# Optimization experiments

Hardware: AMD Instinct MI355X
Metric: run time of the kernel (lower is better)

Reference implementation:

```python
import jax, jax.numpy as jnp
import numpy as np

N = 100000      # nodes
DEG = 16        # fixed out-degree -> nnz = N*DEG (static for jit)
NNZ = N * DEG
IN_DIM, HID, OUT = 256, 64, 64


def setup_inputs() -> dict:
    key = jax.random.key(0)
    k1, k2, k3, k4, k5 = jax.random.split(key, 5)
    X = jax.random.normal(k1, (N, IN_DIM), dtype=jnp.float32)
    W1 = jax.random.normal(k2, (IN_DIM, HID), dtype=jnp.float32) / np.sqrt(IN_DIM)
    W2 = jax.random.normal(k3, (HID, OUT), dtype=jnp.float32) / np.sqrt(HID)
    vals = jax.random.uniform(k4, (NNZ,), dtype=jnp.float32)
    rowptr = (jnp.arange(N + 1, dtype=jnp.int32) * DEG)  # fixed-degree CSR
    colind = jax.random.randint(k5, (NNZ,), 0, N, dtype=jnp.int32)
    return {"X": X, "W1": W1, "W2": W2, "vals": vals,
            "rowptr": rowptr, "colind": colind}


def spmm_csr(rowptr, colind, vals, B):
    """CSR SpMM: out[i] = sum_{j in row i} vals[j] * B[colind[j]]."""
    deg = rowptr[1:] - rowptr[:-1]                      # [N]
    rows = jnp.repeat(jnp.arange(N, dtype=jnp.int32), deg,
                      total_repeat_length=NNZ)           # [NNZ]
    gathered = vals[:, None] * B[colind]                 # [NNZ, F]
    return jax.ops.segment_sum(gathered, rows, num_segments=N)


def reference(X, W1, W2, vals, rowptr, colind):
    h = X @ W1                        # lin1 (no bias)
    h = spmm_csr(rowptr, colind, vals, h)   # A @ h
    h = jax.nn.relu(h)
    out = h @ W2                      # lin2 (no bias)
    out = spmm_csr(rowptr, colind, vals, out)  # A @ out
    return out
```

## Files before the change

### kernel.cpp

```cpp
#include <hip/hip_runtime.h>

#define N_NODES 100000
#define DEG 16

typedef __attribute__((ext_vector_type(8))) short short8;
typedef __attribute__((ext_vector_type(4))) float f32x4;

__device__ inline unsigned short f2bf(float f) {
    union { float f; unsigned u; } v; v.f = f;
    unsigned u = v.u;
    u += 0x7FFFu + ((u >> 16) & 1u);
    return (unsigned short)(u >> 16);
}
__device__ inline float bflo(unsigned u) {
    union { unsigned u; float f; } v; v.u = u << 16; return v.f;
}
__device__ inline float bfhi(unsigned u) {
    union { unsigned u; float f; } v; v.u = u & 0xFFFF0000u; return v.f;
}

__global__ __launch_bounds__(256) void gemm1_k256(const float* __restrict__ X,
                                                  const float* __restrict__ W,
                                                  unsigned short* __restrict__ Y,
                                                  int M)
{
    constexpr int K = 256;
    constexpr int KPAD = K + 8;
    __shared__ unsigned short wfrag[K * 64];
    __shared__ unsigned short stage[4][16 * KPAD];

    const int tid = threadIdx.x;
    for (int idx = tid; idx < K * 64; idx += 256) {
        int j    = idx & 7;
        int lane = (idx >> 3) & 63;
        int ct   = (idx >> 9) & 3;
        int kb   = idx >> 11;
        int k    = kb * 32 + ((lane >> 4) << 3) + j;
        int col  = ct * 16 + (lane & 15);
        wfrag[idx] = f2bf(W[k * 64 + col]);
    }
    __syncthreads();

    const int lane = tid & 63;
    const int wid  = tid >> 6;
    const int q    = lane >> 4;
    const int l16  = lane & 15;
    const int rowbase = blockIdx.x * 64 + wid * 16;
    unsigned short* st = stage[wid];

    #pragma unroll
    for (int r = 0; r < 16; ++r) {
        int rg = rowbase + r; if (rg > M - 1) rg = M - 1;
        float4 x4 = *(const float4*)(X + (size_t)rg * K + lane * 4);
        ushort4 s;
        s.x = f2bf(x4.x); s.y = f2bf(x4.y); s.z = f2bf(x4.z); s.w = f2bf(x4.w);
        *(ushort4*)&st[r * KPAD + lane * 4] = s;
    }

    f32x4 acc0 = {0,0,0,0}, acc1 = {0,0,0,0}, acc2 = {0,0,0,0}, acc3 = {0,0,0,0};
    #pragma unroll
    for (int kb = 0; kb < K / 32; ++kb) {
        short8 af = *(const short8*)&st[l16 * KPAD + kb * 32 + q * 8];
        const short8* wp = (const short8*)&wfrag[((kb * 4) * 64 + lane) * 8];
        acc0 = __builtin_amdgcn_mfma_f32_16x16x32_bf16(af, wp[0 * 64], acc0, 0, 0, 0);
        acc1 = __builtin_amdgcn_mfma_f32_16x16x32_bf16(af, wp[1 * 64], acc1, 0, 0, 0);
        acc2 = __builtin_amdgcn_mfma_f32_16x16x32_bf16(af, wp[2 * 64], acc2, 0, 0, 0);
        acc3 = __builtin_amdgcn_mfma_f32_16x16x32_bf16(af, wp[3 * 64], acc3, 0, 0, 0);
    }

    unsigned short* ob = st;
    #pragma unroll
    for (int r = 0; r < 4; ++r) {
        int rr = (q * 4 + r) * 72 + l16;
        ob[rr + 0 * 16] = f2bf(acc0[r]);
        ob[rr + 1 * 16] = f2bf(acc1[r]);
        ob[rr + 2 * 16] = f2bf(acc2[r]);
        ob[rr + 3 * 16] = f2bf(acc3[r]);
    }
    #pragma unroll
    for (int i = 0; i < 4; ++i) {
        int row = i * 4 + q;
        int rg  = rowbase + row;
        if (rg < M) {
            uint2 v = *(const uint2*)&ob[row * 72 + l16 * 4];
            *(uint2*)(Y + (size_t)rg * 64 + l16 * 4) = v;
        }
    }
}

__global__ __launch_bounds__(256) void gemm2_k64(const unsigned short* __restrict__ Xb,
                                                 const float* __restrict__ W,
                                                 unsigned short* __restrict__ Y,
                                                 int M)
{
    constexpr int K = 64;
    constexpr int KPAD = K + 8;
    __shared__ unsigned short wfrag[K * 64];
    __shared__ unsigned short stage[4][16 * KPAD];

    const int tid = threadIdx.x;
    for (int idx = tid; idx < K * 64; idx += 256) {
        int j    = idx & 7;
        int lane = (idx >> 3) & 63;
        int ct   = (idx >> 9) & 3;
        int kb   = idx >> 11;
        int k    = kb * 32 + ((lane >> 4) << 3) + j;
        int col  = ct * 16 + (lane & 15);
        wfrag[idx] = f2bf(W[k * 64 + col]);
    }
    __syncthreads();

    const int lane = tid & 63;
    const int wid  = tid >> 6;
    const int q    = lane >> 4;
    const int l16  = lane & 15;
    const int rowbase = blockIdx.x * 64 + wid * 16;
    unsigned short* st = stage[wid];

    #pragma unroll
    for (int i = 0; i < 4; ++i) {
        int row = i * 4 + q;
        int rg  = rowbase + row; if (rg > M - 1) rg = M - 1;
        uint2 v = *(const uint2*)(Xb + (size_t)rg * 64 + l16 * 4);
        *(uint2*)&st[row * KPAD + l16 * 4] = v;
    }

    f32x4 acc0 = {0,0,0,0}, acc1 = {0,0,0,0}, acc2 = {0,0,0,0}, acc3 = {0,0,0,0};
    #pragma unroll
    for (int kb = 0; kb < K / 32; ++kb) {
        short8 af = *(const short8*)&st[l16 * KPAD + kb * 32 + q * 8];
        const short8* wp = (const short8*)&wfrag[((kb * 4) * 64 + lane) * 8];
        acc0 = __builtin_amdgcn_mfma_f32_16x16x32_bf16(af, wp[0 * 64], acc0, 0, 0, 0);
        acc1 = __builtin_amdgcn_mfma_f32_16x16x32_bf16(af, wp[1 * 64], acc1, 0, 0, 0);
        acc2 = __builtin_amdgcn_mfma_f32_16x16x32_bf16(af, wp[2 * 64], acc2, 0, 0, 0);
        acc3 = __builtin_amdgcn_mfma_f32_16x16x32_bf16(af, wp[3 * 64], acc3, 0, 0, 0);
    }

    unsigned short* ob = st;
    #pragma unroll
    for (int r = 0; r < 4; ++r) {
        int rr = (q * 4 + r) * 72 + l16;
        ob[rr + 0 * 16] = f2bf(acc0[r]);
        ob[rr + 1 * 16] = f2bf(acc1[r]);
        ob[rr + 2 * 16] = f2bf(acc2[r]);
        ob[rr + 3 * 16] = f2bf(acc3[r]);
    }
    #pragma unroll
    for (int i = 0; i < 4; ++i) {
        int row = i * 4 + q;
        int rg  = rowbase + row;
        if (rg < M) {
            uint2 v = *(const uint2*)&ob[row * 72 + l16 * 4];
            *(uint2*)(Y + (size_t)rg * 64 + l16 * 4) = v;
        }
    }
}

template<bool RELU, bool OUT_BF16>
__global__ __launch_bounds__(256) void spmm16_bf16(const int* __restrict__ colind,
                                                   const float* __restrict__ vals,
                                                   const unsigned short* __restrict__ B,
                                                   void* __restrict__ outp)
{
    const int tid  = threadIdx.x;
    const int lane = tid & 63;
    const int wid  = tid >> 6;
    const int q    = lane >> 4;
    const int l16  = lane & 15;
    const int row  = (blockIdx.x * 4 + wid) * 4 + q;

    const int*   ci = colind + (size_t)row * DEG;
    const float* vv = vals   + (size_t)row * DEG;

    float a0 = 0.f, a1 = 0.f, a2 = 0.f, a3 = 0.f;
    #pragma unroll
    for (int e = 0; e < DEG; ++e) {
        int   c = ci[e];
        float v = vv[e];
        uint2 b = *(const uint2*)(B + (size_t)c * 64 + l16 * 4);
        a0 += v * bflo(b.x); a1 += v * bfhi(b.x);
        a2 += v * bflo(b.y); a3 += v * bfhi(b.y);
    }
    if (RELU) {
        a0 = fmaxf(a0, 0.f); a1 = fmaxf(a1, 0.f);
        a2 = fmaxf(a2, 0.f); a3 = fmaxf(a3, 0.f);
    }
    if (OUT_BF16) {
        ushort4 o; o.x = f2bf(a0); o.y = f2bf(a1); o.z = f2bf(a2); o.w = f2bf(a3);
        *(ushort4*)((unsigned short*)outp + (size_t)row * 64 + l16 * 4) = o;
    } else {
        float4 o; o.x = a0; o.y = a1; o.z = a2; o.w = a3;
        *(float4*)((float*)outp + (size_t)row * 64 + l16 * 4) = o;
    }
}

extern "C" void kernel_launch(void* const* d_in, const int* in_sizes, int n_in,
                              void* d_out, int out_size, void* d_ws, size_t ws_size,
                              hipStream_t stream) {
    const float* X      = (const float*)d_in[0];
    const float* W1     = (const float*)d_in[1];
    const float* W2     = (const float*)d_in[2];
    const float* vals   = (const float*)d_in[3];
    const int*   colind = (const int*)d_in[5];
    float*       out    = (float*)d_out;

    unsigned short* h  = (unsigned short*)d_ws;
    unsigned short* h2 = h + (size_t)N_NODES * 64;
    unsigned short* o1 = h;

    const int gemm_grid = (N_NODES + 63) / 64;

    hipLaunchKernelGGL(gemm1_k256, dim3(gemm_grid), dim3(256), 0, stream, X, W1, h, N_NODES);
    hipLaunchKernelGGL((spmm16_bf16<true, true>), dim3(6250), dim3(256), 0, stream,
                       colind, vals, h, (void*)h2);
    hipLaunchKernelGGL(gemm2_k64, dim3(gemm_grid), dim3(256), 0, stream, h2, W2, o1, N_NODES);
    hipLaunchKernelGGL((spmm16_bf16<false, false>), dim3(6250), dim3(256), 0, stream,
                       colind, vals, o1, (void*)out);
}
```

Before: 267.4 us.

## Fuse first SpMM with second GEMM; make GEMM1 persistent with register prefetch

GEMM1 becomes a persistent grid of 512 blocks, and each wave loops over 16-row tiles while prefetching the next tile of X into registers. This overlaps global loads with the MFMA work and amortises the per-block weight staging. The ReLU SpMM is fused into the GEMM2 kernel, so each block aggregates its 64 rows in registers, writes them to LDS and multiplies by W2 directly. This removes one kernel launch and the round trip of the intermediate h2 through global memory. The cost is 16 float4 registers of prefetch per thread, which can lower occupancy.

```diff
diff --git a/kernel.cpp b/kernel.cpp
--- a/kernel.cpp
+++ b/kernel.cpp
@@ -2,6 +2,9 @@
 
 #define N_NODES 100000
 #define DEG 16
+#define NT1 6250
+#define G1_BLOCKS 512
+#define G1_WSTRIDE (G1_BLOCKS * 4)
 
 typedef __attribute__((ext_vector_type(8))) short short8;
 typedef __attribute__((ext_vector_type(4))) float f32x4;
@@ -19,24 +22,23 @@
     union { unsigned u; float f; } v; v.u = u & 0xFFFF0000u; return v.f;
 }
 
-__global__ __launch_bounds__(256) void gemm1_k256(const float* __restrict__ X,
-                                                  const float* __restrict__ W,
-                                                  unsigned short* __restrict__ Y,
-                                                  int M)
+__global__ __launch_bounds__(256, 2) void gemm1_k256(const float* __restrict__ X,
+                                                     const float* __restrict__ W,
+                                                     unsigned short* __restrict__ Y)
 {
     constexpr int K = 256;
-    constexpr int KPAD = K + 8;
+    constexpr int KPAD = 264;
     __shared__ unsigned short wfrag[K * 64];
     __shared__ unsigned short stage[4][16 * KPAD];
 
     const int tid = threadIdx.x;
     for (int idx = tid; idx < K * 64; idx += 256) {
         int j    = idx & 7;
-        int lane = (idx >> 3) & 63;
+        int ln   = (idx >> 3) & 63;
         int ct   = (idx >> 9) & 3;
         int kb   = idx >> 11;
-        int k    = kb * 32 + ((lane >> 4) << 3) + j;
-        int col  = ct * 16 + (lane & 15);
+        int k    = kb * 32 + ((ln >> 4) << 3) + j;
+        int col  = ct * 16 + (ln & 15);
         wfrag[idx] = f2bf(W[k * 64 + col]);
     }
     __syncthreads();
@@ -45,122 +47,147 @@
     const int wid  = tid >> 6;
     const int q    = lane >> 4;
     const int l16  = lane & 15;
-    const int rowbase = blockIdx.x * 64 + wid * 16;
     unsigned short* st = stage[wid];
 
-    #pragma unroll
-    for (int r = 0; r < 16; ++r) {
-        int rg = rowbase + r; if (rg > M - 1) rg = M - 1;
-        float4 x4 = *(const float4*)(X + (size_t)rg * K + lane * 4);
+    int t = blockIdx.x * 4 + wid;
+    float4 pf[16];
+    {
+        const float* xb = X + (size_t)t * 16 * K + lane * 4;
+        #pragma unroll
+        for (int r = 0; r < 16; ++r) pf[r] = *(const float4*)(xb + (size_t)r * K);
+    }
+
+    while (t < NT1) {
+        ushort4 cv[16];
+        #pragma unroll
+        for (int r = 0; r < 16; ++r) {
+            cv[r].x = f2bf(pf[r].x); cv[r].y = f2bf(pf[r].y);
+            cv[r].z = f2bf(pf[r].z); cv[r].w = f2bf(pf[r].w);
+        }
+        int tn = t + G1_WSTRIDE;
+        if (tn < NT1) {
+            const float* xb = X + (size_t)tn * 16 * K + lane * 4;
+            #pragma unroll
+            for (int r = 0; r < 16; ++r) pf[r] = *(const float4*)(xb + (size_t)r * K);
+        }
+        #pragma unroll
+        for (int r = 0; r < 16; ++r)
+            *(ushort4*)&st[r * KPAD + lane * 4] = cv[r];
+
+        f32x4 acc0 = {0,0,0,0}, acc1 = {0,0,0,0}, acc2 = {0,0,0,0}, acc3 = {0,0,0,0};
+        #pragma unroll
+        for (int kb = 0; kb < K / 32; ++kb) {
+            short8 af = *(const short8*)&st[l16 * KPAD + kb * 32 + q * 8];
+            const short8* wp = (const short8*)&wfrag[(size_t)((kb * 4) * 64 + lane) * 8];
+            acc0 = __builtin_amdgcn_mfma_f32_16x16x32_bf16(af, wp[0 * 64], acc0, 0, 0, 0);
+            acc1 = __builtin_amdgcn_mfma_f32_16x16x32_bf16(af, wp[1 * 64], acc1, 0, 0, 0);
+            acc2 = __builtin_amdgcn_mfma_f32_16x16x32_bf16(af, wp[2 * 64], acc2, 0, 0, 0);
+            acc3 = __builtin_amdgcn_mfma_f32_16x16x32_bf16(af, wp[3 * 64], acc3, 0, 0, 0);
+        }
+
+        #pragma unroll
+        for (int r = 0; r < 4; ++r) {
+            int rr = (q * 4 + r) * 72 + l16;
+            st[rr + 0 * 16] = f2bf(acc0[r]);
+            st[rr + 1 * 16] = f2bf(acc1[r]);
+            st[rr + 2 * 16] = f2bf(acc2[r]);
+            st[rr + 3 * 16] = f2bf(acc3[r]);
+        }
+        const int rowbase = t * 16;
+        #pragma unroll
+        for (int i = 0; i < 4; ++i) {
+            int row = i * 4 + q;
+            uint2 v = *(const uint2*)&st[row * 72 + l16 * 4];
+            *(uint2*)(Y + (size_t)(rowbase + row) * 64 + l16 * 4) = v;
+        }
+        t = tn;
+    }
+}
+
+__global__ __launch_bounds__(256) void spmm_gemm2(const int* __restrict__ colind,
+                                                  const float* __restrict__ vals,
+                                                  const unsigned short* __restrict__ Bh,
+                                                  const float* __restrict__ W2,
+                                                  unsigned short* __restrict__ Y)
+{
+    constexpr int K = 64;
+    constexpr int KPAD = 72;
+    __shared__ unsigned short wfrag[K * 64];
+    __shared__ unsigned short stage[4][16 * KPAD];
+
+    const int tid = threadIdx.x;
+    for (int idx = tid; idx < K * 64; idx += 256) {
+        int j    = idx & 7;
+        int ln   = (idx >> 3) & 63;
+        int ct   = (idx >> 9) & 3;
+        int kb   = idx >> 11;
+        int k    = kb * 32 + ((ln >> 4) << 3) + j;
+        int col  = ct * 16 + (ln & 15);
+        wfrag[idx] = f2bf(W2[k * 64 + col]);
+    }
+    __syncthreads();
+
+    const int lane = tid & 63;
+    const int wid  = tid >> 6;
+    const int q    = lane >> 4;
+    const int l16  = lane & 15;
+    unsigned short* st = stage[wid];
+    const int base = blockIdx.x * 64 + wid * 16;
+
+    for (int i = 0; i < 4; ++i) {
+        int row = base + i * 4 + q;
+        int rc  = row < N_NODES ? row : N_NODES - 1;
+        const int*   ci = colind + (size_t)rc * DEG;
+        const float* vv = vals   + (size_t)rc * DEG;
+        float a0 = 0.f, a1 = 0.f, a2 = 0.f, a3 = 0.f;
+        #pragma unroll
+        for (int e = 0; e < DEG; ++e) {
+            int   c = ci[e];
+            float v = vv[e];
+            uint2 b = *(const uint2*)(Bh + (size_t)c * 64 + l16 * 4);
+            a0 += v * bflo(b.x); a1 += v * bfhi(b.x);
+            a2 += v * bflo(b.y); a3 += v * bfhi(b.y);
+        }
+        a0 = fmaxf(a0, 0.f); a1 = fmaxf(a1, 0.f);
+        a2 = fmaxf(a2, 0.f); a3 = fmaxf(a3, 0.f);
         ushort4 s;
-        s.x = f2bf(x4.x); s.y = f2bf(x4.y); s.z = f2bf(x4.z); s.w = f2bf(x4.w);
-        *(ushort4*)&st[r * KPAD + lane * 4] = s;
+        s.x = f2bf(a0); s.y = f2bf(a1); s.z = f2bf(a2); s.w = f2bf(a3);
+        *(ushort4*)&st[(i * 4 + q) * KPAD + l16 * 4] = s;
     }
 
     f32x4 acc0 = {0,0,0,0}, acc1 = {0,0,0,0}, acc2 = {0,0,0,0}, acc3 = {0,0,0,0};
     #pragma unroll
     for (int kb = 0; kb < K / 32; ++kb) {
         short8 af = *(const short8*)&st[l16 * KPAD + kb * 32 + q * 8];
-        const short8* wp = (const short8*)&wfrag[((kb * 4) * 64 + lane) * 8];
+        const short8* wp = (const short8*)&wfrag[(size_t)((kb * 4) * 64 + lane) * 8];
         acc0 = __builtin_amdgcn_mfma_f32_16x16x32_bf16(af, wp[0 * 64], acc0, 0, 0, 0);
         acc1 = __builtin_amdgcn_mfma_f32_16x16x32_bf16(af, wp[1 * 64], acc1, 0, 0, 0);
         acc2 = __builtin_amdgcn_mfma_f32_16x16x32_bf16(af, wp[2 * 64], acc2, 0, 0, 0);
         acc3 = __builtin_amdgcn_mfma_f32_16x16x32_bf16(af, wp[3 * 64], acc3, 0, 0, 0);
     }
 
-    unsigned short* ob = st;
     #pragma unroll
     for (int r = 0; r < 4; ++r) {
-        int rr = (q * 4 + r) * 72 + l16;
-        ob[rr + 0 * 16] = f2bf(acc0[r]);
-        ob[rr + 1 * 16] = f2bf(acc1[r]);
-        ob[rr + 2 * 16] = f2bf(acc2[r]);
-        ob[rr + 3 * 16] = f2bf(acc3[r]);
+        int rr = (q * 4 + r) * KPAD + l16;
+        st[rr + 0 * 16] = f2bf(acc0[r]);
+        st[rr + 1 * 16] = f2bf(acc1[r]);
+        st[rr + 2 * 16] = f2bf(acc2[r]);
+        st[rr + 3 * 16] = f2bf(acc3[r]);
     }
     #pragma unroll
     for (int i = 0; i < 4; ++i) {
-        int row = i * 4 + q;
-        int rg  = rowbase + row;
-        if (rg < M) {
-            uint2 v = *(const uint2*)&ob[row * 72 + l16 * 4];
-            *(uint2*)(Y + (size_t)rg * 64 + l16 * 4) = v;
-        }
-    }
-}
-
-__global__ __launch_bounds__(256) void gemm2_k64(const unsigned short* __restrict__ Xb,
-                                                 const float* __restrict__ W,
-                                                 unsigned short* __restrict__ Y,
-                                                 int M)
-{
-    constexpr int K = 64;
-    constexpr int KPAD = K + 8;
-    __shared__ unsigned short wfrag[K * 64];
-    __shared__ unsigned short stage[4][16 * KPAD];
-
-    const int tid = threadIdx.x;
-    for (int idx = tid; idx < K * 64; idx += 256) {
-        int j    = idx & 7;
-        int lane = (idx >> 3) & 63;
-        int ct   = (idx >> 9) & 3;
-        int kb   = idx >> 11;
-        int k    = kb * 32 + ((lane >> 4) << 3) + j;
-        int col  = ct * 16 + (lane & 15);
-        wfrag[idx] = f2bf(W[k * 64 + col]);
-    }
-    __syncthreads();
-
-    const int lane = tid & 63;
-    const int wid  = tid >> 6;
-    const int q    = lane >> 4;
-    const int l16  = lane & 15;
-    const int rowbase = blockIdx.x * 64 + wid * 16;
-    unsigned short* st = stage[wid];
-
-    #pragma unroll
-    for (int i = 0; i < 4; ++i) {
-        int row = i * 4 + q;
-        int rg  = rowbase + row; if (rg > M - 1) rg = M - 1;
-        uint2 v = *(const uint2*)(Xb + (size_t)rg * 64 + l16 * 4);
-        *(uint2*)&st[row * KPAD + l16 * 4] = v;
-    }
-
-    f32x4 acc0 = {0,0,0,0}, acc1 = {0,0,0,0}, acc2 = {0,0,0,0}, acc3 = {0,0,0,0};
-    #pragma unroll
-    for (int kb = 0; kb < K / 32; ++kb) {
-        short8 af = *(const short8*)&st[l16 * KPAD + kb * 32 + q * 8];
-        const short8* wp = (const short8*)&wfrag[((kb * 4) * 64 + lane) * 8];
-        acc0 = __builtin_amdgcn_mfma_f32_16x16x32_bf16(af, wp[0 * 64], acc0, 0, 0, 0);
-        acc1 = __builtin_amdgcn_mfma_f32_16x16x32_bf16(af, wp[1 * 64], acc1, 0, 0, 0);
-        acc2 = __builtin_amdgcn_mfma_f32_16x16x32_bf16(af, wp[2 * 64], acc2, 0, 0, 0);
-        acc3 = __builtin_amdgcn_mfma_f32_16x16x32_bf16(af, wp[3 * 64], acc3, 0, 0, 0);
-    }
-
-    unsigned short* ob = st;
-    #pragma unroll
-    for (int r = 0; r < 4; ++r) {
-        int rr = (q * 4 + r) * 72 + l16;
-        ob[rr + 0 * 16] = f2bf(acc0[r]);
-        ob[rr + 1 * 16] = f2bf(acc1[r]);
-        ob[rr + 2 * 16] = f2bf(acc2[r]);
-        ob[rr + 3 * 16] = f2bf(acc3[r]);
-    }
-    #pragma unroll
-    for (int i = 0; i < 4; ++i) {
-        int row = i * 4 + q;
-        int rg  = rowbase + row;
-        if (rg < M) {
-            uint2 v = *(const uint2*)&ob[row * 72 + l16 * 4];
-            *(uint2*)(Y + (size_t)rg * 64 + l16 * 4) = v;
-        }
-    }
-}
-
-template<bool RELU, bool OUT_BF16>
-__global__ __launch_bounds__(256) void spmm16_bf16(const int* __restrict__ colind,
-                                                   const float* __restrict__ vals,
-                                                   const unsigned short* __restrict__ B,
-                                                   void* __restrict__ outp)
+        int row = base + i * 4 + q;
+        if (row < N_NODES) {
+            uint2 v = *(const uint2*)&st[(i * 4 + q) * KPAD + l16 * 4];
+            *(uint2*)(Y + (size_t)row * 64 + l16 * 4) = v;
+        }
+    }
+}
+
+__global__ __launch_bounds__(256) void spmm_out(const int* __restrict__ colind,
+                                                const float* __restrict__ vals,
+                                                const unsigned short* __restrict__ B,
+                                                float* __restrict__ out)
 {
     const int tid  = threadIdx.x;
     const int lane = tid & 63;
@@ -181,17 +208,8 @@
         a0 += v * bflo(b.x); a1 += v * bfhi(b.x);
         a2 += v * bflo(b.y); a3 += v * bfhi(b.y);
     }
-    if (RELU) {
-        a0 = fmaxf(a0, 0.f); a1 = fmaxf(a1, 0.f);
-        a2 = fmaxf(a2, 0.f); a3 = fmaxf(a3, 0.f);
-    }
-    if (OUT_BF16) {
-        ushort4 o; o.x = f2bf(a0); o.y = f2bf(a1); o.z = f2bf(a2); o.w = f2bf(a3);
-        *(ushort4*)((unsigned short*)outp + (size_t)row * 64 + l16 * 4) = o;
-    } else {
-        float4 o; o.x = a0; o.y = a1; o.z = a2; o.w = a3;
-        *(float4*)((float*)outp + (size_t)row * 64 + l16 * 4) = o;
-    }
+    float4 o; o.x = a0; o.y = a1; o.z = a2; o.w = a3;
+    *(float4*)(out + (size_t)row * 64 + l16 * 4) = o;
 }
 
 extern "C" void kernel_launch(void* const* d_in, const int* in_sizes, int n_in,
@@ -205,15 +223,11 @@
     float*       out    = (float*)d_out;
 
     unsigned short* h  = (unsigned short*)d_ws;
-    unsigned short* h2 = h + (size_t)N_NODES * 64;
-    unsigned short* o1 = h;
-
-    const int gemm_grid = (N_NODES + 63) / 64;
-
-    hipLaunchKernelGGL(gemm1_k256, dim3(gemm_grid), dim3(256), 0, stream, X, W1, h, N_NODES);
-    hipLaunchKernelGGL((spmm16_bf16<true, true>), dim3(6250), dim3(256), 0, stream,
-                       colind, vals, h, (void*)h2);
-    hipLaunchKernelGGL(gemm2_k64, dim3(gemm_grid), dim3(256), 0, stream, h2, W2, o1, N_NODES);
-    hipLaunchKernelGGL((spmm16_bf16<false, false>), dim3(6250), dim3(256), 0, stream,
-                       colind, vals, o1, (void*)out);
-}
+    unsigned short* o1 = h + (size_t)N_NODES * 64;
+
+    hipLaunchKernelGGL(gemm1_k256, dim3(G1_BLOCKS), dim3(256), 0, stream, X, W1, h);
+    hipLaunchKernelGGL(spmm_gemm2, dim3((N_NODES + 63) / 64), dim3(256), 0, stream,
+                       colind, vals, h, W2, o1);
+    hipLaunchKernelGGL(spmm_out, dim3(N_NODES / 16), dim3(256), 0, stream,
+                       colind, vals, o1, out);
+}
```

New measurement: 251.0 us. -6.1%, faster.
